# Optimization experiments

Hardware: AMD Instinct MI355X
Metric: run time of the kernel (lower is better)

## Reference

```python
import jax, jax.numpy as jnp
import numpy as np

BETA = 0.99  # EMA momentum from init_kwargs
EPS = 1e-12  # torch F.normalize eps


def _normalize(v):
    # matches torch.nn.functional.normalize (L2, dim=-1, eps clamp)
    n = jnp.maximum(jnp.linalg.norm(v, axis=-1, keepdims=True), EPS)
    return v / n


def setup_inputs() -> dict:
    key = jax.random.key(0)
    k1, k2 = jax.random.split(key)
    x = jax.random.normal(k1, (16384, 1024), dtype=jnp.float32)
    group_features = jax.random.uniform(k2, (8192, 1024), dtype=jnp.float32)
    return {"x": x, "group_features": group_features}


def reference(x, group_features):
    n_groups = group_features.shape[0]
    # assign_groups: cosine-sim argmax (normalized copies; does NOT modify x used below)
    xn = _normalize(x)
    gn = _normalize(group_features)
    logits = xn @ gn.T                      # [B, G]
    assignments = jnp.argmax(logits, axis=-1)  # [B] int

    # bincount over groups
    counts = jax.ops.segment_sum(
        jnp.ones_like(assignments, dtype=jnp.int32), assignments, num_segments=n_groups
    )  # [G]

    # scale only groups that received at least one sample by beta
    gf = jnp.where((counts > 0)[:, None], group_features * BETA, group_features)

    # scatter-add EMA contribution: (1-beta) * mean-style sum of raw x per group
    per_sample = x / counts[assignments][:, None].astype(x.dtype)  # safe: count>=1 for assigned
    contrib = jax.ops.segment_sum(per_sample, assignments, num_segments=n_groups)  # [G, D]
    gf = gf + (1.0 - BETA) * contrib

    return _normalize(gf)
```

## Files before the change

### kernel.cpp

```cpp
#include <hip/hip_runtime.h>

#define B_N 16384
#define G_N 8192
#define D_N 1024
#define NT 96

typedef unsigned short u16;
typedef unsigned long long u64;
typedef __attribute__((ext_vector_type(8))) short short8;
typedef __attribute__((ext_vector_type(16))) float f32x16;

#define AS1 __attribute__((address_space(1)))
#define AS3 __attribute__((address_space(3)))


__global__ __launch_bounds__(256) void k_norms(const float* __restrict__ g,
                                               float* __restrict__ invn) {
    const int j = blockIdx.x;
    const int t = threadIdx.x;
    const float4 v = *reinterpret_cast<const float4*>(&g[(size_t)j * D_N + t * 4]);
    float s = v.x * v.x + v.y * v.y + v.z * v.z + v.w * v.w;
#pragma unroll
    for (int off = 32; off >= 1; off >>= 1) s += __shfl_down(s, off, 64);
    __shared__ float wsum[4];
    if ((t & 63) == 0) wsum[t >> 6] = s;
    __syncthreads();
    if (t == 0) {
        const float tot = wsum[0] + wsum[1] + wsum[2] + wsum[3];
        invn[j] = 1.0f / fmaxf(sqrtf(tot), 1e-12f);
    }
}

__global__ void k_counts(const u64* __restrict__ pk, int* __restrict__ counts) {
    const int i = blockIdx.x * blockDim.x + threadIdx.x;
    if (i < B_N) {
        const int a = 8191 - (int)(pk[i] & 0x1FFFull);
        atomicAdd(&counts[a], 1);
    }
}

__global__ __launch_bounds__(256) void k_scatter(const float* __restrict__ x,
                                                 const u64* __restrict__ pk,
                                                 const int* __restrict__ counts,
                                                 float* __restrict__ contrib) {
    const int i = blockIdx.x;
    const int a = 8191 - (int)(pk[i] & 0x1FFFull);
    const float scale = 1.0f / (float)counts[a];
    const int t = threadIdx.x;
    const float4 v = *reinterpret_cast<const float4*>(&x[(size_t)i * D_N + t * 4]);
    float* dst = &contrib[(size_t)a * D_N + t * 4];
    atomicAdd(dst + 0, v.x * scale);
    atomicAdd(dst + 1, v.y * scale);
    atomicAdd(dst + 2, v.z * scale);
    atomicAdd(dst + 3, v.w * scale);
}

__global__ __launch_bounds__(256) void k_finalize(const float* __restrict__ g,
                                                  const int* __restrict__ counts,
                                                  float* __restrict__ out) {
    const int j = blockIdx.x;
    const int t = threadIdx.x;
    const float sc = (counts[j] > 0) ? 0.99f : 1.0f;
    const float4 gv = *reinterpret_cast<const float4*>(&g[(size_t)j * D_N + t * 4]);
    const float4 cv = *reinterpret_cast<const float4*>(&out[(size_t)j * D_N + t * 4]);
    float4 gf;
    gf.x = sc * gv.x + 0.01f * cv.x;
    gf.y = sc * gv.y + 0.01f * cv.y;
    gf.z = sc * gv.z + 0.01f * cv.z;
    gf.w = sc * gv.w + 0.01f * cv.w;
    float s = gf.x * gf.x + gf.y * gf.y + gf.z * gf.z + gf.w * gf.w;
#pragma unroll
    for (int off = 32; off >= 1; off >>= 1) s += __shfl_down(s, off, 64);
    __shared__ float wsum[4];
    __shared__ float s_inv;
    if ((t & 63) == 0) wsum[t >> 6] = s;
    __syncthreads();
    if (t == 0) s_inv = 1.0f / fmaxf(sqrtf(wsum[0] + wsum[1] + wsum[2] + wsum[3]), 1e-12f);
    __syncthreads();
    gf.x *= s_inv; gf.y *= s_inv; gf.z *= s_inv; gf.w *= s_inv;
    *reinterpret_cast<float4*>(&out[(size_t)j * D_N + t * 4]) = gf;
}


__device__ inline u16 f2bf_rtn(float f) {
    unsigned u = __float_as_uint(f);
    unsigned r = u + 0x7fffu + ((u >> 16) & 1u);
    return (u16)(r >> 16);
}
__device__ inline float bf2f(u16 h) { return __uint_as_float(((unsigned)h) << 16); }

__global__ __launch_bounds__(256) void k_split_pack(const float* __restrict__ src,
                                                    u16* __restrict__ hi,
                                                    u16* __restrict__ lo) {
    const int id = blockIdx.x * 256 + threadIdx.x;
    const int brick = id >> 7, c = id & 127;
    const int mu = brick >> 5, tau = brick & 31;
    const int ks = c >> 6, lane = c & 63;
    const int row = mu * 32 + (lane & 31);
    const int k = tau * 32 + ks * 16 + (lane >> 5) * 8;
    const float* s = src + (size_t)row * D_N + k;
    const float4 v0 = *reinterpret_cast<const float4*>(s);
    const float4 v1 = *reinterpret_cast<const float4*>(s + 4);
    const float f[8] = {v0.x, v0.y, v0.z, v0.w, v1.x, v1.y, v1.z, v1.w};
    short8 h, l;
#pragma unroll
    for (int j = 0; j < 8; ++j) {
        const u16 hj = f2bf_rtn(f[j]);
        h[j] = (short)hj;
        l[j] = (short)f2bf_rtn(f[j] - bf2f(hj));
    }
    *reinterpret_cast<short8*>(hi + (size_t)id * 8) = h;
    *reinterpret_cast<short8*>(lo + (size_t)id * 8) = l;
}


#define MFMA_BLK(S) do {                                                                   \
    _Pragma("unroll")                                                                      \
    for (int ks = 0; ks < 2; ++ks)                                                         \
        _Pragma("unroll")                                                                  \
        for (int m = 0; m < 4; ++m)                                                        \
            _Pragma("unroll")                                                              \
            for (int n = 0; n < 2; ++n)                                                    \
                acc[m][n] = __builtin_amdgcn_mfma_f32_32x32x16_bf16(                       \
                    afr[S][m][ks], bfr[S][n][ks], acc[S][m][ks], 0, 0, 0);                 \
} while (0)

#undef MFMA_BLK
#define MFMA_BLK(S) do {                                                                   \
    _Pragma("unroll")                                                                      \
    for (int ks = 0; ks < 2; ++ks)                                                         \
        _Pragma("unroll")                                                                  \
        for (int m = 0; m < 4; ++m)                                                        \
            _Pragma("unroll")                                                              \
            for (int n = 0; n < 2; ++n)                                                    \
                acc[m][n] = __builtin_amdgcn_mfma_f32_32x32x16_bf16(                       \
                    afr[S][m][ks], bfr[S][n][ks], acc[m][n], 0, 0, 0);                     \
} while (0)

#define READS(BUF, S) do {                                                                 \
    const u16* aB = lds + (BUF) * 16384 + aRd;                                             \
    const u16* bB = lds + (BUF) * 16384 + 8192 + bRd;                                      \
    _Pragma("unroll")                                                                      \
    for (int m = 0; m < 4; ++m)                                                            \
        _Pragma("unroll")                                                                  \
        for (int ks = 0; ks < 2; ++ks)                                                     \
            afr[S][m][ks] = *reinterpret_cast<const short8*>(aB + m * 1024 + ks * 512);    \
    _Pragma("unroll")                                                                      \
    for (int n = 0; n < 2; ++n)                                                            \
        _Pragma("unroll")                                                                  \
        for (int ks = 0; ks < 2; ++ks)                                                     \
            bfr[S][n][ks] = *reinterpret_cast<const short8*>(bB + n * 1024 + ks * 512);    \
} while (0)

#define SGB __builtin_amdgcn_sched_group_barrier

#define BODY(P, BSTG, BRD, SM, SR) do {                                                    \
    asm volatile("s_waitcnt vmcnt(4)" ::: "memory");                                       \
    __builtin_amdgcn_s_barrier();                                                          \
    STG((P) + 3, BSTG);                                                                    \
    READS(BRD, SR);                                                                        \
    __builtin_amdgcn_s_setprio(1);                                                         \
    MFMA_BLK(SM);                                                                          \
    __builtin_amdgcn_s_setprio(0);                                                         \
    _Pragma("unroll")                                                                      \
    for (int q = 0; q < 12; ++q) { SGB(0x100, 1, 0); SGB(0x008, 1, 0); }                   \
    SGB(0x008, 4, 0);                                                                      \
    SGB(0x070, 4, 0);                                                                      \
} while (0)

__global__ __launch_bounds__(512, 2) void k_gemm_argmax(
    const u16* __restrict__ x_hi, const u16* __restrict__ x_lo,
    const u16* __restrict__ g_hi, const u16* __restrict__ g_lo,
    const float* __restrict__ invn, u64* __restrict__ pk) {

    __shared__ __align__(16) u16 lds[65536];

    const int bid = blockIdx.x;
    const int xcd = bid & 7, lcl = bid >> 3;
    const int mblk = xcd * 8 + ((lcl >> 3) & 7);
    const int nblk = (lcl & 7) + (lcl >> 6) * 8;
    const int mrow0 = mblk * 256, nrow0 = nblk * 256;

    const int tid = threadIdx.x;
    const int lane = tid & 63;
    const int w = tid >> 6;
    const int wr = w >> 2, wc = w & 3;
    const int l31 = lane & 31, l5 = lane >> 5;

    const int aRd = (wr * 512 + lane) * 8;
    const int bRd = (wc * 256 + lane) * 8;

    const int wub = (tid & 448) * 8;
    const int cOff = (tid & 127) * 8;
    const int brkA = tid >> 7;
    const size_t aBase = ((size_t)(mblk * 8 + brkA)) * 32768 + cOff;
    const size_t bBase = ((size_t)(nblk * 8 + brkA)) * 32768 + cOff;

    auto STG = [&](int T, int buf) {
        const int Tc = T < NT ? T : NT - 1;
        const int term = Tc >> 5;
        const int tko = (Tc & 31) * 1024;
        const u16* xa = ((term == 1) ? x_lo : x_hi) + aBase + tko;
        const u16* gb = ((term == 2) ? g_lo : g_hi) + bBase + tko;
        u16* da = lds + buf * 16384 + wub;
        u16* db = da + 8192;
        __builtin_amdgcn_global_load_lds((const AS1 void*)xa,            (AS3 void*)da, 16, 0, 0);
        __builtin_amdgcn_global_load_lds((const AS1 void*)(xa + 131072), (AS3 void*)(da + 4096), 16, 0, 0);
        __builtin_amdgcn_global_load_lds((const AS1 void*)gb,            (AS3 void*)db, 16, 0, 0);
        __builtin_amdgcn_global_load_lds((const AS1 void*)(gb + 131072), (AS3 void*)(db + 4096), 16, 0, 0);
    };

    f32x16 acc[4][2];
#pragma unroll
    for (int m = 0; m < 4; ++m)
#pragma unroll
        for (int n = 0; n < 2; ++n)
#pragma unroll
            for (int r = 0; r < 16; ++r) acc[m][n][r] = 0.0f;

    short8 afr[2][4][2], bfr[2][2][2];

    STG(0, 0); STG(1, 1); STG(2, 2);
    asm volatile("s_waitcnt vmcnt(8)" ::: "memory");
    __builtin_amdgcn_s_barrier();
    READS(0, 0);

    for (int it = 0; it < 24; ++it) {
        const int p = it * 4;
        BODY(p,     3, 1, 0, 1);
        BODY(p + 1, 0, 2, 1, 0);
        BODY(p + 2, 1, 3, 0, 1);
        BODY(p + 3, 2, 0, 1, 0);
    }

    float inv[2];
    inv[0] = invn[nrow0 + wc * 64 + l31];
    inv[1] = invn[nrow0 + wc * 64 + 32 + l31];

#pragma unroll
    for (int m = 0; m < 4; ++m) {
#pragma unroll
        for (int r = 0; r < 16; ++r) {
            u64 p = 0;
#pragma unroll
            for (int n = 0; n < 2; ++n) {
                const float v = acc[m][n][r] * inv[n];
                unsigned u = __float_as_uint(v);
                u ^= (u >> 31) ? 0xFFFFFFFFu : 0x80000000u;
                const int col = nrow0 + wc * 64 + n * 32 + l31;
                const u64 cand = ((u64)u << 13) | (unsigned)(8191 - col);
                p = (cand > p) ? cand : p;
            }
#pragma unroll
            for (int msk = 1; msk < 32; msk <<= 1) {
                const u64 o = __shfl_xor(p, msk, 64);
                p = (o > p) ? o : p;
            }
            if (l31 == 0) {
                const int row = mrow0 + wr * 128 + m * 32 + (r & 3) + 8 * (r >> 2) + 4 * l5;
                atomicMax(&pk[row], p);
            }
        }
    }
}


__global__ __launch_bounds__(256) void k_argmax_fp32(const float* __restrict__ x,
                                                     const float* __restrict__ g,
                                                     const float* __restrict__ invn,
                                                     int* __restrict__ assign) {
    __shared__ __align__(16) float As[32][68];
    __shared__ __align__(16) float Bs[32][68];
    const int t = threadIdx.x;
    const int tx = t & 15;
    const int ty = t >> 4;
    const int row0 = blockIdx.x * 64;
    const int r_a = t >> 3;
    const int c4 = t & 7;
    float bestv[4]; int besti[4];
#pragma unroll
    for (int i = 0; i < 4; ++i) { bestv[i] = -3.0e38f; besti[i] = 0; }
    for (int jt = 0; jt < G_N / 64; ++jt) {
        float acc[4][4] = {};
        for (int kt = 0; kt < D_N / 32; ++kt) {
#pragma unroll
            for (int p = 0; p < 2; ++p) {
                const int r = r_a + p * 32;
                const float4 va = *reinterpret_cast<const float4*>(&x[(size_t)(row0 + r) * D_N + kt * 32 + c4 * 4]);
                As[c4 * 4 + 0][r] = va.x; As[c4 * 4 + 1][r] = va.y; As[c4 * 4 + 2][r] = va.z; As[c4 * 4 + 3][r] = va.w;
                const float4 vb = *reinterpret_cast<const float4*>(&g[(size_t)(jt * 64 + r) * D_N + kt * 32 + c4 * 4]);
                Bs[c4 * 4 + 0][r] = vb.x; Bs[c4 * 4 + 1][r] = vb.y; Bs[c4 * 4 + 2][r] = vb.z; Bs[c4 * 4 + 3][r] = vb.w;
            }
            __syncthreads();
#pragma unroll
            for (int k = 0; k < 32; ++k) {
                const float4 a = *reinterpret_cast<const float4*>(&As[k][ty * 4]);
                const float4 b = *reinterpret_cast<const float4*>(&Bs[k][tx * 4]);
                const float av[4] = {a.x, a.y, a.z, a.w};
                const float bv[4] = {b.x, b.y, b.z, b.w};
#pragma unroll
                for (int i = 0; i < 4; ++i)
#pragma unroll
                    for (int jj = 0; jj < 4; ++jj) acc[i][jj] += av[i] * bv[jj];
            }
            __syncthreads();
        }
#pragma unroll
        for (int jj = 0; jj < 4; ++jj) {
            const int col = jt * 64 + tx * 4 + jj;
            const float s = invn[col];
#pragma unroll
            for (int i = 0; i < 4; ++i) {
                const float v = acc[i][jj] * s;
                if (v > bestv[i]) { bestv[i] = v; besti[i] = col; }
            }
        }
    }
#pragma unroll
    for (int m = 1; m < 16; m <<= 1) {
#pragma unroll
        for (int i = 0; i < 4; ++i) {
            const float ov = __shfl_xor(bestv[i], m, 64);
            const int oi = __shfl_xor(besti[i], m, 64);
            if (ov > bestv[i] || (ov == bestv[i] && oi < besti[i])) { bestv[i] = ov; besti[i] = oi; }
        }
    }
    if (tx == 0) {
#pragma unroll
        for (int i = 0; i < 4; ++i) assign[row0 + ty * 4 + i] = besti[i];
    }
}

__global__ void k_counts_i(const int* __restrict__ assign, int* __restrict__ counts) {
    const int i = blockIdx.x * blockDim.x + threadIdx.x;
    if (i < B_N) atomicAdd(&counts[assign[i]], 1);
}

__global__ __launch_bounds__(256) void k_scatter_i(const float* __restrict__ x,
                                                   const int* __restrict__ assign,
                                                   const int* __restrict__ counts,
                                                   float* __restrict__ contrib) {
    const int i = blockIdx.x;
    const int a = assign[i];
    const float scale = 1.0f / (float)counts[a];
    const int t = threadIdx.x;
    const float4 v = *reinterpret_cast<const float4*>(&x[(size_t)i * D_N + t * 4]);
    float* dst = &contrib[(size_t)a * D_N + t * 4];
    atomicAdd(dst + 0, v.x * scale);
    atomicAdd(dst + 1, v.y * scale);
    atomicAdd(dst + 2, v.z * scale);
    atomicAdd(dst + 3, v.w * scale);
}


extern "C" void kernel_launch(void* const* d_in, const int* in_sizes, int n_in,
                              void* d_out, int out_size, void* d_ws, size_t ws_size,
                              hipStream_t stream) {
    const float* x = (const float*)d_in[0];
    const float* g = (const float*)d_in[1];
    float* out = (float*)d_out;

    char* ws = (char*)d_ws;
    u16*  x_hi  = (u16*)(ws);
    u16*  x_lo  = (u16*)(ws + 33554432);
    u16*  g_hi  = (u16*)(ws + 67108864);
    u16*  g_lo  = (u16*)(ws + 83886080);
    float* invn = (float*)(ws + 100663296);
    int* counts = (int*)(ws + 100696064);
    u64*   pk   = (u64*)(ws + 100728832);
    const size_t need = 100859904;

    hipMemsetAsync(out, 0, (size_t)G_N * D_N * sizeof(float), stream);

    if (ws_size >= need) {
        hipMemsetAsync(counts, 0, (size_t)G_N * sizeof(int), stream);
        hipMemsetAsync(pk, 0, (size_t)B_N * sizeof(u64), stream);
        k_norms<<<G_N, 256, 0, stream>>>(g, invn);
        k_split_pack<<<B_N * D_N / 8 / 256, 256, 0, stream>>>(x, x_hi, x_lo);
        k_split_pack<<<G_N * D_N / 8 / 256, 256, 0, stream>>>(g, g_hi, g_lo);
        k_gemm_argmax<<<2048, 512, 0, stream>>>(x_hi, x_lo, g_hi, g_lo, invn, pk);
        k_counts<<<B_N / 256, 256, 0, stream>>>(pk, counts);
        k_scatter<<<B_N, 256, 0, stream>>>(x, pk, counts, out);
        k_finalize<<<G_N, 256, 0, stream>>>(g, counts, out);
    } else {
        float* invn_f = (float*)ws;
        int* assign_f = (int*)(ws + (size_t)G_N * 4);
        int* counts_f = (int*)(ws + (size_t)(G_N + B_N) * 4);
        hipMemsetAsync(counts_f, 0, (size_t)G_N * sizeof(int), stream);
        k_norms<<<G_N, 256, 0, stream>>>(g, invn_f);
        k_argmax_fp32<<<B_N / 64, 256, 0, stream>>>(x, g, invn_f, assign_f);
        k_counts_i<<<B_N / 256, 256, 0, stream>>>(assign_f, counts_f);
        k_scatter_i<<<B_N, 256, 0, stream>>>(x, assign_f, counts_f, out);
        k_finalize<<<G_N, 256, 0, stream>>>(g, counts_f, out);
    }
}
```

Baseline: 1.027 ms.

## Load GEMM B fragments directly from global into registers, halve LDS

The G operand is no longer staged through LDS. Each wave loads its own B fragments straight from global memory into registers one stage ahead. Only the X operand still goes through global_load_lds, which halves the LDS footprint and the LDS read traffic. The explicit sched_group_barrier interleaving is removed. In exchange, waves that share a column each fetch the same B data from global/L2, and B load latency now falls on register dependencies right before the MFMAs.

```diff
diff --git a/kernel.cpp b/kernel.cpp
--- a/kernel.cpp
+++ b/kernel.cpp
@@ -115,18 +115,7 @@
 
 
 #define MFMA_BLK(S) do {                                                                   \
-    _Pragma("unroll")                                                                      \
-    for (int ks = 0; ks < 2; ++ks)                                                         \
-        _Pragma("unroll")                                                                  \
-        for (int m = 0; m < 4; ++m)                                                        \
-            _Pragma("unroll")                                                              \
-            for (int n = 0; n < 2; ++n)                                                    \
-                acc[m][n] = __builtin_amdgcn_mfma_f32_32x32x16_bf16(                       \
-                    afr[S][m][ks], bfr[S][n][ks], acc[S][m][ks], 0, 0, 0);                 \
-} while (0)
-
-#undef MFMA_BLK
-#define MFMA_BLK(S) do {                                                                   \
+    __builtin_amdgcn_s_setprio(1);                                                         \
     _Pragma("unroll")                                                                      \
     for (int ks = 0; ks < 2; ++ks)                                                         \
         _Pragma("unroll")                                                                  \
@@ -135,37 +124,34 @@
             for (int n = 0; n < 2; ++n)                                                    \
                 acc[m][n] = __builtin_amdgcn_mfma_f32_32x32x16_bf16(                       \
                     afr[S][m][ks], bfr[S][n][ks], acc[m][n], 0, 0, 0);                     \
+    __builtin_amdgcn_s_setprio(0);                                                         \
 } while (0)
 
-#define READS(BUF, S) do {                                                                 \
-    const u16* aB = lds + (BUF) * 16384 + aRd;                                             \
-    const u16* bB = lds + (BUF) * 16384 + 8192 + bRd;                                      \
+#define READS_A(BUF, S) do {                                                               \
+    const u16* aB = lds + (BUF) * 8192 + aRd;                                              \
     _Pragma("unroll")                                                                      \
     for (int m = 0; m < 4; ++m)                                                            \
         _Pragma("unroll")                                                                  \
         for (int ks = 0; ks < 2; ++ks)                                                     \
             afr[S][m][ks] = *reinterpret_cast<const short8*>(aB + m * 1024 + ks * 512);    \
-    _Pragma("unroll")                                                                      \
-    for (int n = 0; n < 2; ++n)                                                            \
-        _Pragma("unroll")                                                                  \
-        for (int ks = 0; ks < 2; ++ks)                                                     \
-            bfr[S][n][ks] = *reinterpret_cast<const short8*>(bB + n * 1024 + ks * 512);    \
 } while (0)
 
-#define SGB __builtin_amdgcn_sched_group_barrier
+#define BLOAD(T, S) do {                                                                   \
+    const int Tc_ = (T) < NT ? (T) : NT - 1;                                               \
+    const u16* gp = (((Tc_ >> 5) == 2) ? g_lo : g_hi) + bGlob + (size_t)(Tc_ & 31) * 1024; \
+    bfr[S][0][0] = *reinterpret_cast<const short8*>(gp);                                   \
+    bfr[S][0][1] = *reinterpret_cast<const short8*>(gp + 512);                             \
+    bfr[S][1][0] = *reinterpret_cast<const short8*>(gp + 32768);                           \
+    bfr[S][1][1] = *reinterpret_cast<const short8*>(gp + 32768 + 512);                     \
+} while (0)
 
 #define BODY(P, BSTG, BRD, SM, SR) do {                                                    \
-    asm volatile("s_waitcnt vmcnt(4)" ::: "memory");                                       \
+    asm volatile("s_waitcnt vmcnt(6)" ::: "memory");                                       \
     __builtin_amdgcn_s_barrier();                                                          \
-    STG((P) + 3, BSTG);                                                                    \
-    READS(BRD, SR);                                                                        \
-    __builtin_amdgcn_s_setprio(1);                                                         \
+    STG_A((P) + 3, BSTG);                                                                  \
+    BLOAD((P) + 1, SR);                                                                    \
+    READS_A(BRD, SR);                                                                      \
     MFMA_BLK(SM);                                                                          \
-    __builtin_amdgcn_s_setprio(0);                                                         \
-    _Pragma("unroll")                                                                      \
-    for (int q = 0; q < 12; ++q) { SGB(0x100, 1, 0); SGB(0x008, 1, 0); }                   \
-    SGB(0x008, 4, 0);                                                                      \
-    SGB(0x070, 4, 0);                                                                      \
 } while (0)
 
 __global__ __launch_bounds__(512, 2) void k_gemm_argmax(
@@ -173,7 +159,7 @@
     const u16* __restrict__ g_hi, const u16* __restrict__ g_lo,
     const float* __restrict__ invn, u64* __restrict__ pk) {
 
-    __shared__ __align__(16) u16 lds[65536];
+    __shared__ __align__(16) u16 lds[32768];
 
     const int bid = blockIdx.x;
     const int xcd = bid & 7, lcl = bid >> 3;
@@ -187,27 +173,23 @@
     const int wr = w >> 2, wc = w & 3;
     const int l31 = lane & 31, l5 = lane >> 5;
 
-    const int aRd = (wr * 512 + lane) * 8;
-    const int bRd = (wc * 256 + lane) * 8;
+    const int aRd = wr * 4096 + lane * 8;
+
+    const size_t bGlob = ((size_t)(nblk * 8 + wc * 2)) * 32768 + (size_t)lane * 8;
 
     const int wub = (tid & 448) * 8;
     const int cOff = (tid & 127) * 8;
     const int brkA = tid >> 7;
     const size_t aBase = ((size_t)(mblk * 8 + brkA)) * 32768 + cOff;
-    const size_t bBase = ((size_t)(nblk * 8 + brkA)) * 32768 + cOff;
-
-    auto STG = [&](int T, int buf) {
+
+    auto STG_A = [&](int T, int buf) {
         const int Tc = T < NT ? T : NT - 1;
         const int term = Tc >> 5;
         const int tko = (Tc & 31) * 1024;
         const u16* xa = ((term == 1) ? x_lo : x_hi) + aBase + tko;
-        const u16* gb = ((term == 2) ? g_lo : g_hi) + bBase + tko;
-        u16* da = lds + buf * 16384 + wub;
-        u16* db = da + 8192;
+        u16* da = lds + buf * 8192 + wub;
         __builtin_amdgcn_global_load_lds((const AS1 void*)xa,            (AS3 void*)da, 16, 0, 0);
         __builtin_amdgcn_global_load_lds((const AS1 void*)(xa + 131072), (AS3 void*)(da + 4096), 16, 0, 0);
-        __builtin_amdgcn_global_load_lds((const AS1 void*)gb,            (AS3 void*)db, 16, 0, 0);
-        __builtin_amdgcn_global_load_lds((const AS1 void*)(gb + 131072), (AS3 void*)(db + 4096), 16, 0, 0);
     };
 
     f32x16 acc[4][2];
@@ -220,10 +202,11 @@
 
     short8 afr[2][4][2], bfr[2][2][2];
 
-    STG(0, 0); STG(1, 1); STG(2, 2);
+    STG_A(0, 0); STG_A(1, 1); STG_A(2, 2);
+    BLOAD(0, 0);
     asm volatile("s_waitcnt vmcnt(8)" ::: "memory");
     __builtin_amdgcn_s_barrier();
-    READS(0, 0);
+    READS_A(0, 0);
 
     for (int it = 0; it < 24; ++it) {
         const int p = it * 4;
```

After: 1.123 ms, median of 2. +9.4%, slower.
